# Kernel optimization log

Measured on AMD Instinct MI355X. Metric: run time of the kernel, lower is better.

## Reference

```python
import jax, jax.numpy as jnp
import numpy as np
import math

H, W = 1024, 1024

def setup_inputs() -> dict:
    key = jax.random.key(0)
    img = jax.random.uniform(key, (H, W), dtype=jnp.float32) * 255.0
    return {"InputImage": img}

def _phase_congruency(img):
    nrows, ncols = img.shape
    minWaveLength, mult = 3.0, 2.1
    nscale, norient = 5, 6
    sigmaOnf, k, cutOff, g = 0.55, 2.0, 0.5, 10.0
    eps = 1e-4

    cy, cx = nrows // 2, ncols // 2
    yy, xx = jnp.mgrid[0:nrows, 0:ncols]
    yy = (yy - cy) / nrows
    xx = (xx - cx) / ncols
    radius = jnp.sqrt(xx ** 2 + yy ** 2)
    radius = radius.at[cy, cx].set(1.0)
    theta = jnp.arctan2(-yy, xx)
    sintheta, costheta = jnp.sin(theta), jnp.cos(theta)

    # low-pass Butterworth (order 15, cutoff 0.45)
    normradius = radius / (jnp.abs(xx).max() * 2)
    lowpass = 1.0 / (1.0 + (normradius / 0.45) ** 30)

    # log-Gabor radial filters, [nscale, H, W]
    s = jnp.arange(nscale, dtype=jnp.float32)
    fo = 1.0 / (minWaveLength * mult ** s)            # [S]
    logGabor = jnp.exp(-jnp.log(radius[None] * (1.0 / fo)[:, None, None]) ** 2
                       / (2 * math.log(sigmaOnf) ** 2))
    annular = logGabor * lowpass[None]
    annular = annular.at[:, cy, cx].set(0.0)

    # angular spread, [norient, H, W]
    angl = jnp.arange(norient, dtype=jnp.float32) * (math.pi / norient)
    cosA, sinA = jnp.cos(angl), jnp.sin(angl)
    ds = sintheta[None] * cosA[:, None, None] - costheta[None] * sinA[:, None, None]
    dc = costheta[None] * cosA[:, None, None] + sintheta[None] * sinA[:, None, None]
    dtheta = jnp.minimum(jnp.abs(jnp.arctan2(ds, dc)) * (norient / 2), math.pi)
    spread = (jnp.cos(dtheta) + 1.0) / 2.0

    # full filter bank [O, S, H, W], shifted to DFT layout
    filt = jnp.fft.ifftshift(spread[:, None] * annular[None], axes=(-2, -1))

    F = jnp.fft.fft2(img)                              # complex64
    # cv2.idft is unscaled -> multiply numpy-style ifft by N
    z = jnp.fft.ifft2(filt * F[None, None]) * (nrows * ncols)   # [O,S,H,W]
    # original code: E (even) = channel 1 = Im(z), O (odd) = channel 0 = Re(z)
    E, O = z.imag, z.real
    An = jnp.abs(z)

    sumE = E.sum(axis=1)        # [O,H,W]
    sumO = O.sum(axis=1)
    sumAn = An.sum(axis=1)
    maxAn = An.max(axis=1)
    tau = jnp.median(An[:, 0].reshape(norient, -1), axis=1) / math.sqrt(math.log(4.0))

    XEnergy = jnp.sqrt(sumE ** 2 + sumO ** 2) + eps
    MeanE = sumE / XEnergy
    MeanO = sumO / XEnergy
    Energy = (E * MeanE[:, None] + O * MeanO[:, None]
              - jnp.abs(E * MeanO[:, None] - O * MeanE[:, None])).sum(axis=1)

    totalTau = tau * (1 - (1 / mult) ** nscale) / (1 - 1 / mult)   # [O]
    T = totalTau * math.sqrt(math.pi / 2) + k * totalTau * math.sqrt((4 - math.pi) / 2)
    Energy = jnp.maximum(Energy - T[:, None, None], 0.0)

    width = (sumAn / (maxAn + eps) - 1.0) / (nscale - 1)
    weight = 1.0 / (1.0 + jnp.exp((cutOff - width) * g))
    PC = weight * Energy / sumAn                       # [O,H,W]

    covx = PC * cosA[:, None, None]
    covy = PC * sinA[:, None, None]
    covx2 = (covx ** 2).sum(axis=0) / (norient / 2)
    covy2 = (covy ** 2).sum(axis=0) / (norient / 2)
    covxy = 4.0 * (covx * covy).sum(axis=0) / norient
    denom = jnp.sqrt(covxy ** 2 + (covx2 - covy2) ** 2) + eps
    M = (covy2 + covx2 + denom) / 2.0
    m = (covy2 + covx2 - denom) / 2.0
    return M, m

def reference(InputImage):
    M, m = _phase_congruency(InputImage)
    return (M, m)
```

## Files before the change

kernel.cpp:

```cpp
#include <hip/hip_runtime.h>
#include <math.h>

typedef float2 c2;

#define S_IDX(i) ((i) ^ (((i) >> 5) & 15))
#define SLAB_STRIDE 1025

__device__ __forceinline__ c2 cmul(c2 a, c2 b){
  return make_float2(a.x*b.x - a.y*b.y, a.x*b.y + a.y*b.x);
}

__constant__ float c_foinv[5] = {3.0f, 6.3f, 13.23f, 27.783f, 58.3443f};
__constant__ float c_lnfo[5]  = {1.0986123f, 1.8405496f, 2.5824700f, 3.3244106f, 4.0663219f};
__constant__ float c_angl[6]  = {0.0f, 0.5235988f, 1.0471976f, 1.5707963f, 2.0943951f, 2.6179939f};
__constant__ float c_cosA[6] = {1.0f, 0.8660254038f, 0.5f, 6.123233996e-17f, -0.5f, -0.8660254038f};
__constant__ float c_sinA[6] = {0.0f, 0.5f, 0.8660254038f, 1.0f, 0.8660254038f, 0.5f};

template<int SIGN>
__device__ __forceinline__ void make_tw(int t, c2* w){
#pragma unroll
  for (int k = 0; k < 5; ++k){
    const int s = 1 << (2*k);
    const float ang = (float)SIGN * 0.00613592315154256f * (float)(t & ~(s-1));
    sincosf(ang, &w[k].y, &w[k].x);
  }
}

template<int SIGN>
__device__ __forceinline__ void fft1024(c2* bufA, c2* bufB, int t, const c2* w){
  c2* cur = bufA; c2* oth = bufB;
#pragma unroll
  for (int k = 0; k < 5; ++k){
    const int s = 1 << (2*k);
    const int q = t & (s - 1);
    c2 a = cur[S_IDX(t)];
    c2 b = cur[S_IDX(t + 256)];
    c2 c = cur[S_IDX(t + 512)];
    c2 d = cur[S_IDX(t + 768)];
    c2 w1 = w[k];
    c2 w2 = cmul(w1, w1);
    c2 w3 = cmul(w2, w1);
    c2 apc = make_float2(a.x + c.x, a.y + c.y);
    c2 amc = make_float2(a.x - c.x, a.y - c.y);
    c2 bpd = make_float2(b.x + d.x, b.y + d.y);
    c2 bmd = make_float2(b.x - d.x, b.y - d.y);
    c2 y0 = make_float2(apc.x + bpd.x, apc.y + bpd.y);
    c2 e2 = make_float2(apc.x - bpd.x, apc.y - bpd.y);
    const float S4 = (float)SIGN;
    c2 u1 = make_float2(amc.x - S4*bmd.y, amc.y + S4*bmd.x);
    c2 u3 = make_float2(amc.x + S4*bmd.y, amc.y - S4*bmd.x);
    c2 y1 = cmul(u1, w1);
    c2 y2 = cmul(e2, w2);
    c2 y3 = cmul(u3, w3);
    const int bw = 4*t - 3*q;
    oth[S_IDX(bw)]       = y0;
    oth[S_IDX(bw + s)]   = y1;
    oth[S_IDX(bw + 2*s)] = y2;
    oth[S_IDX(bw + 3*s)] = y3;
    c2* tmp = cur; cur = oth; oth = tmp;
    __syncthreads();
  }
}

__device__ __forceinline__ float filt_eval(int c, int r, float yy,
                                           float cosA, float sinA, float foinv){
  const float xx = (float)(c < 512 ? c : c - 1024) * (1.0f/1024.0f);
  const bool isdc = (c == 0) && (r == 0);
  const float radius = isdc ? 1.0f : sqrtf(xx*xx + yy*yy);
  const float tt = radius * (1.0f/0.45f);
  const float t2 = tt*tt, t4 = t2*t2, t8 = t4*t4, t16 = t8*t8;
  const float lp = 1.0f / (1.0f + t16*t8*t4*t2);
  const float lnr = logf(radius * foinv);
  const float lg = expf(-lnr*lnr * 1.3989572f);
  const float ir = 1.0f / radius;
  const float st = -yy * ir, ct = xx * ir;
  const float dsv = st*cosA - ct*sinA;
  const float dcv = ct*cosA + st*sinA;
  const float dth = fminf(fabsf(atan2f(dsv, dcv)) * 3.0f, 3.14159274f);
  const float spr = 0.5f * (cosf(dth) + 1.0f);
  const float f = lg * lp * spr;
  return isdc ? 0.0f : f;
}

__global__ __launch_bounds__(256) void k_filt_tab(float* __restrict__ lnrT, float* __restrict__ thetaT){
  const int r = blockIdx.x;
  const int t = threadIdx.x;
  const float yy = (float)(r < 512 ? r : r - 1024) * (1.0f/1024.0f);
#pragma unroll
  for (int j = 0; j < 4; ++j){
    const int c = t + 256*j;
    const float xx = (float)(c < 512 ? c : c - 1024) * (1.0f/1024.0f);
    const float radius = sqrtf(xx*xx + yy*yy);
    float lnr = logf(radius);
    if (r == 0 && c == 0) lnr = __int_as_float(0x7F800000);
    lnrT[r*1024 + c] = lnr;
    thetaT[r*1024 + c] = atan2f(-yy, xx);
  }
}

__global__ __launch_bounds__(256) void k_fft_fwd_real(const float* __restrict__ in, c2* __restrict__ out){
  const int t = threadIdx.x;
  __shared__ c2 bufA[1024];
  __shared__ c2 bufB[1024];
  c2 w[5]; make_tw<-1>(t, w);
  for (int rr = 0; rr < 4; ++rr){
    const int row = blockIdx.x * 4 + rr;
    const float* src = in + (size_t)row * 1024;
    c2* dst = out + (size_t)row * 1024;
#pragma unroll
    for (int j = 0; j < 4; ++j){
      const int q = t + 256*j;
      bufA[S_IDX(q)] = make_float2(src[q], 0.0f);
    }
    __syncthreads();
    fft1024<-1>(bufA, bufB, t, w);
#pragma unroll
    for (int j = 0; j < 4; ++j){ const int q = t + 256*j; dst[q] = bufB[S_IDX(q)]; }
    __syncthreads();
  }
}

template<int SIGN>
__global__ __launch_bounds__(256) void k_fft_col_slab(c2* __restrict__ Z){
  __shared__ c2 slab[8 * SLAB_STRIDE];
  __shared__ c2 bufB[1024];
  c2* base = Z + (size_t)blockIdx.y * 1048576;
  const int t = threadIdx.x;
  const int col0 = blockIdx.x * 8;
  const int cl = t & 7;
  const int rw = t >> 3;
  c2 w[5]; make_tw<SIGN>(t, w);
  for (int ch = 0; ch < 32; ++ch){
    const int row = ch * 32 + rw;
    slab[cl * SLAB_STRIDE + S_IDX(row)] = base[(size_t)row * 1024 + col0 + cl];
  }
  __syncthreads();
  for (int c = 0; c < 8; ++c){
    c2* colp = slab + c * SLAB_STRIDE;
#pragma unroll
    for (int j = 0; j < 4; ++j) bufB[t + 256*j] = colp[t + 256*j];
    __syncthreads();
    fft1024<SIGN>(bufB, colp, t, w);
  }
  for (int ch = 0; ch < 32; ++ch){
    const int row = ch * 32 + rw;
    base[(size_t)row * 1024 + col0 + cl] = slab[cl * SLAB_STRIDE + S_IDX(row)];
  }
}

__global__ __launch_bounds__(256) void k_fft_inv_filter_t(const c2* __restrict__ F, c2* __restrict__ Z,
                                                          const float* __restrict__ lnrT,
                                                          const float* __restrict__ thetaT){
  const int t = threadIdx.x;
  const int gslot = blockIdx.y;
  const int orient = gslot / 5;
  const int scale = gslot - orient*5;
  const float lnfo = c_lnfo[scale];
  const float angl = c_angl[orient];
  __shared__ c2 bufA[1024];
  __shared__ c2 bufB[1024];
  c2 w[5]; make_tw<1>(t, w);
  for (int rr = 0; rr < 4; ++rr){
    const int row = blockIdx.x * 4 + rr;
    const c2* src = F + (size_t)row * 1024;
    const float* lnrR = lnrT + (size_t)row * 1024;
    const float* thR  = thetaT + (size_t)row * 1024;
    c2* dst = Z + (size_t)gslot * 1048576 + (size_t)row * 1024;
#pragma unroll
    for (int j = 0; j < 4; ++j){
      const int q = t + 256*j;
      const c2 v = src[q];
      const float lnr = lnrR[q];
      const float th  = thR[q];
      const float u = lnr + lnfo;
      const float lg = __expf(-u*u * 1.3989572f);
      const float lp = 1.0f / (1.0f + __expf(fmaf(30.0f, lnr, 23.955231f)));
      float d = th - angl;
      if (d <= -3.14159274f) d += 6.28318548f;
      const float dth = fminf(fabsf(d) * 3.0f, 3.14159274f);
      const float spr = 0.5f * (__cosf(dth) + 1.0f);
      const float f = lg * lp * spr;
      bufA[S_IDX(q)] = make_float2(v.x*f, v.y*f);
    }
    __syncthreads();
    fft1024<1>(bufA, bufB, t, w);
#pragma unroll
    for (int j = 0; j < 4; ++j){ const int q = t + 256*j; dst[q] = bufB[S_IDX(q)]; }
    __syncthreads();
  }
}

__global__ __launch_bounds__(256) void k_fft_inv_filter_b(const c2* __restrict__ F, c2* __restrict__ Z,
                                                          int slot0){
  const int t = threadIdx.x;
  const int gslot = slot0 + blockIdx.y;
  const int orient = gslot / 5;
  const int scale = gslot - orient*5;
  const float foinv = c_foinv[scale];
  const float cosA = c_cosA[orient], sinA = c_sinA[orient];
  __shared__ c2 bufA[1024];
  __shared__ c2 bufB[1024];
  c2 w[5]; make_tw<1>(t, w);
  for (int rr = 0; rr < 4; ++rr){
    const int row = blockIdx.x * 4 + rr;
    const c2* src = F + (size_t)row * 1024;
    c2* dst = Z + (size_t)blockIdx.y * 1048576 + (size_t)row * 1024;
    const float yy = (float)(row < 512 ? row : row - 1024) * (1.0f/1024.0f);
#pragma unroll
    for (int j = 0; j < 4; ++j){
      const int q = t + 256*j;
      const c2 v = src[q];
      const float f = filt_eval(q, row, yy, cosA, sinA, foinv);
      bufA[S_IDX(q)] = make_float2(v.x*f, v.y*f);
    }
    __syncthreads();
    fft1024<1>(bufA, bufB, t, w);
#pragma unroll
    for (int j = 0; j < 4; ++j){ const int q = t + 256*j; dst[q] = bufB[S_IDX(q)]; }
    __syncthreads();
  }
}


__device__ __forceinline__ unsigned amp_bits(const c2 v){
  return __float_as_uint(sqrtf(v.x*v.x + v.y*v.y));
}

__global__ __launch_bounds__(256) void k_med_p1b(const c2* __restrict__ Zb, size_t oStride,
                                                 unsigned* __restrict__ g1, int oBase){
  __shared__ unsigned h[4][4096];
  const int t = threadIdx.x;
  const int wv = t >> 6;
  const c2* z0 = Zb + (size_t)blockIdx.y * oStride;
  unsigned* gg = g1 + (size_t)(oBase + blockIdx.y) * 4096;
  for (int j = t; j < 4*4096; j += 256) ((unsigned*)h)[j] = 0;
  __syncthreads();
  const int base = blockIdx.x * 16384;
  for (int it = 0; it < 64; ++it){
    const unsigned bits = amp_bits(z0[base + it*256 + t]);
    atomicAdd(&h[wv][bits >> 20], 1u);
  }
  __syncthreads();
  for (int j = t; j < 4096; j += 256){
    const unsigned s = h[0][j] + h[1][j] + h[2][j] + h[3][j];
    if (s) atomicAdd(&gg[j], s);
  }
}

__global__ __launch_bounds__(256) void k_sel1b(const unsigned* __restrict__ g1,
                                               unsigned* __restrict__ sc1,
                                               unsigned* __restrict__ g2, int oBase){
  __shared__ unsigned partial[256];
  const int t = threadIdx.x;
  const int oo = oBase + blockIdx.x;
  const unsigned* gg = g1 + (size_t)oo * 4096;
  unsigned loc[16]; unsigned s = 0;
#pragma unroll
  for (int j = 0; j < 16; ++j){ loc[j] = gg[t*16 + j]; s += loc[j]; }
  partial[t] = s;
  __syncthreads();
  unsigned p = 0;
  for (int u = 0; u < t; ++u) p += partial[u];
  for (int which = 0; which < 2; ++which){
    const unsigned R = 524287u + (unsigned)which;
    if (R >= p && R - p < s){
      unsigned cum = p;
      for (int j = 0; j < 16; ++j){
        if (R - cum < loc[j]){ sc1[oo*4 + which*2] = (unsigned)(t*16 + j); sc1[oo*4 + which*2+1] = R - cum; break; }
        cum += loc[j];
      }
    }
  }
  for (int j = t; j < 8192; j += 256) g2[(size_t)oo*8192 + j] = 0;
}

__global__ __launch_bounds__(256) void k_med_p2b(const c2* __restrict__ Zb, size_t oStride,
                                                 const unsigned* __restrict__ sc1,
                                                 unsigned* __restrict__ g2, int oBase){
  __shared__ unsigned h[2][4096];
  const int t = threadIdx.x;
  const int oo = oBase + blockIdx.y;
  const c2* z0 = Zb + (size_t)blockIdx.y * oStride;
  unsigned* gg = g2 + (size_t)oo * 8192;
  for (int j = t; j < 8192; j += 256) ((unsigned*)h)[j] = 0;
  __syncthreads();
  const unsigned b0 = sc1[oo*4 + 0], b1 = sc1[oo*4 + 2];
  const int base = blockIdx.x * 16384;
  for (int it = 0; it < 64; ++it){
    const unsigned bits = amp_bits(z0[base + it*256 + t]);
    const unsigned top = bits >> 20;
    const unsigned mid = (bits >> 8) & 4095u;
    if (top == b0)      atomicAdd(&h[0][mid], 1u);
    else if (top == b1) atomicAdd(&h[1][mid], 1u);
  }
  __syncthreads();
  for (int j = t; j < 4096; j += 256){
    if (h[0][j]) atomicAdd(&gg[j], h[0][j]);
    if (h[1][j]) atomicAdd(&gg[4096 + j], h[1][j]);
  }
}

__global__ __launch_bounds__(256) void k_sel2b(const unsigned* __restrict__ g2,
                                               const unsigned* __restrict__ sc1,
                                               unsigned* __restrict__ sc2,
                                               unsigned* __restrict__ g3, int oBase){
  __shared__ unsigned partial[256];
  const int t = threadIdx.x;
  const int oo = oBase + blockIdx.x;
  const unsigned b0 = sc1[oo*4+0], lr0 = sc1[oo*4+1], b1 = sc1[oo*4+2], lr1 = sc1[oo*4+3];
  for (int which = 0; which < 2; ++which){
    const unsigned* hh = g2 + (size_t)oo*8192 + ((which == 1 && b1 != b0) ? 4096 : 0);
    const unsigned R = which ? lr1 : lr0;
    unsigned loc[16]; unsigned s = 0;
#pragma unroll
    for (int j = 0; j < 16; ++j){ loc[j] = hh[t*16 + j]; s += loc[j]; }
    partial[t] = s;
    __syncthreads();
    unsigned p = 0;
    for (int u = 0; u < t; ++u) p += partial[u];
    if (R >= p && R - p < s){
      unsigned cum = p;
      for (int j = 0; j < 16; ++j){
        if (R - cum < loc[j]){ sc2[oo*4 + which*2] = (unsigned)(t*16 + j); sc2[oo*4 + which*2+1] = R - cum; break; }
        cum += loc[j];
      }
    }
    __syncthreads();
  }
  for (int j = t; j < 512; j += 256) g3[(size_t)oo*512 + j] = 0;
}

__global__ __launch_bounds__(256) void k_med_p3b(const c2* __restrict__ Zb, size_t oStride,
                                                 const unsigned* __restrict__ sc1,
                                                 const unsigned* __restrict__ sc2,
                                                 unsigned* __restrict__ g3, int oBase){
  __shared__ unsigned h[2][256];
  const int t = threadIdx.x;
  const int oo = oBase + blockIdx.y;
  const c2* z0 = Zb + (size_t)blockIdx.y * oStride;
  unsigned* gg = g3 + (size_t)oo * 512;
  h[0][t] = 0; h[1][t] = 0;
  __syncthreads();
  const unsigned k0 = (sc1[oo*4+0] << 12) | sc2[oo*4+0];
  const unsigned k1 = (sc1[oo*4+2] << 12) | sc2[oo*4+2];
  const int base = blockIdx.x * 16384;
  for (int it = 0; it < 64; ++it){
    const unsigned bits = amp_bits(z0[base + it*256 + t]);
    const unsigned key = bits >> 8;
    if (key == k0)       atomicAdd(&h[0][bits & 255u], 1u);
    else if (key == k1)  atomicAdd(&h[1][bits & 255u], 1u);
  }
  __syncthreads();
  if (h[0][t]) atomicAdd(&gg[t], h[0][t]);
  if (h[1][t]) atomicAdd(&gg[256 + t], h[1][t]);
}

__global__ __launch_bounds__(256) void k_sel3b(const unsigned* __restrict__ g3,
                                               const unsigned* __restrict__ sc1,
                                               const unsigned* __restrict__ sc2,
                                               float* __restrict__ Tval, int oBase){
  __shared__ unsigned partial[256];
  __shared__ float vres[2];
  const int t = threadIdx.x;
  const int oo = oBase + blockIdx.x;
  const unsigned k0 = (sc1[oo*4+0] << 12) | sc2[oo*4+0];
  const unsigned k1 = (sc1[oo*4+2] << 12) | sc2[oo*4+2];
  for (int which = 0; which < 2; ++which){
    const unsigned* hh = g3 + (size_t)oo*512 + ((which == 1 && k1 != k0) ? 256 : 0);
    const unsigned R = which ? sc2[oo*4+3] : sc2[oo*4+1];
    partial[t] = hh[t];
    __syncthreads();
    unsigned p = 0;
    for (int u = 0; u < t; ++u) p += partial[u];
    if (R >= p && R - p < partial[t]){
      const unsigned key = which ? k1 : k0;
      vres[which] = __uint_as_float((key << 8) | (unsigned)t);
    }
    __syncthreads();
  }
  if (t == 0){
    const float med = 0.5f * (vres[0] + vres[1]);
    const float tau = med / 1.17741001f;
    const float totalTau = tau * 1.8623464f;
    const float T = totalTau * 1.25331414f + 2.0f * totalTau * 0.65513638f;
    Tval[oo] = T;
  }
}


__global__ __launch_bounds__(256) void k_pix_all(const c2* __restrict__ Z, const float* __restrict__ Tval,
                                                 float* __restrict__ out){
  const int i = blockIdx.x * 256 + threadIdx.x;
  float covx2 = 0.f, covy2 = 0.f, covxy = 0.f;
#pragma unroll
  for (int o = 0; o < 6; ++o){
    const float T = Tval[o];
    float E[5], O[5];
    float sumE = 0.f, sumO = 0.f, sumAn = 0.f, maxAn = 0.f;
#pragma unroll
    for (int s = 0; s < 5; ++s){
      const c2 z = Z[(size_t)(o*5 + s) * 1048576 + i];
      O[s] = z.x; E[s] = z.y;
      const float an = sqrtf(z.x*z.x + z.y*z.y);
      sumE += E[s]; sumO += O[s]; sumAn += an; maxAn = fmaxf(maxAn, an);
    }
    const float XE = sqrtf(sumE*sumE + sumO*sumO) + 1e-4f;
    const float ME = sumE / XE, MO = sumO / XE;
    float energy = 0.f;
#pragma unroll
    for (int s = 0; s < 5; ++s)
      energy += E[s]*ME + O[s]*MO - fabsf(E[s]*MO - O[s]*ME);
    energy = fmaxf(energy - T, 0.f);
    const float width = (sumAn / (maxAn + 1e-4f) - 1.0f) * 0.25f;
    const float weight = 1.0f / (1.0f + expf((0.5f - width) * 10.0f));
    const float PC = weight * energy / sumAn;
    const float cx = PC * c_cosA[o], cy = PC * c_sinA[o];
    covx2 += cx*cx; covy2 += cy*cy; covxy += cx*cy;
  }
  covx2 *= (1.0f/3.0f);
  covy2 *= (1.0f/3.0f);
  covxy *= (4.0f/6.0f);
  const float dnm = sqrtf(covxy*covxy + (covx2 - covy2)*(covx2 - covy2)) + 1e-4f;
  const float ss = covy2 + covx2;
  out[i] = (ss + dnm) / 2.0f;
  out[1048576 + i] = (ss - dnm) / 2.0f;
}


__global__ __launch_bounds__(256) void k_pix(const c2* __restrict__ Z, const float* __restrict__ Tp,
                                             float cA, float sA,
                                             float* __restrict__ ax2, float* __restrict__ ay2,
                                             float* __restrict__ axy, int first){
  const int i = blockIdx.x * 256 + threadIdx.x;
  const float T = *Tp;
  float E[5], O[5];
  float sumE = 0.f, sumO = 0.f, sumAn = 0.f, maxAn = 0.f;
#pragma unroll
  for (int s = 0; s < 5; ++s){
    const c2 z = Z[(size_t)s * 1048576 + i];
    O[s] = z.x; E[s] = z.y;
    const float an = sqrtf(z.x*z.x + z.y*z.y);
    sumE += E[s]; sumO += O[s]; sumAn += an; maxAn = fmaxf(maxAn, an);
  }
  const float XE = sqrtf(sumE*sumE + sumO*sumO) + 1e-4f;
  const float ME = sumE / XE, MO = sumO / XE;
  float energy = 0.f;
#pragma unroll
  for (int s = 0; s < 5; ++s)
    energy += E[s]*ME + O[s]*MO - fabsf(E[s]*MO - O[s]*ME);
  energy = fmaxf(energy - T, 0.f);
  const float width = (sumAn / (maxAn + 1e-4f) - 1.0f) * 0.25f;
  const float weight = 1.0f / (1.0f + expf((0.5f - width) * 10.0f));
  const float PC = weight * energy / sumAn;
  const float cx = PC * cA, cy = PC * sA;
  if (first){ ax2[i] = cx*cx; ay2[i] = cy*cy; axy[i] = cx*cy; }
  else      { ax2[i] += cx*cx; ay2[i] += cy*cy; axy[i] += cx*cy; }
}

__global__ __launch_bounds__(256) void k_final(const float* __restrict__ ax2, const float* __restrict__ ay2,
                                               const float* __restrict__ axy, float* __restrict__ out){
  const int i = blockIdx.x * 256 + threadIdx.x;
  const float cx2 = ax2[i] / 3.0f;
  const float cy2 = ay2[i] / 3.0f;
  const float cxy = 4.0f * axy[i] / 6.0f;
  const float dnm = sqrtf(cxy*cxy + (cx2 - cy2)*(cx2 - cy2)) + 1e-4f;
  const float ss = cy2 + cx2;
  out[i] = (ss + dnm) / 2.0f;
  out[1048576 + i] = (ss - dnm) / 2.0f;
}

extern "C" void kernel_launch(void* const* d_in, const int* in_sizes, int n_in,
                              void* d_out, int out_size, void* d_ws, size_t ws_size,
                              hipStream_t stream){
  (void)in_sizes; (void)n_in; (void)out_size;
  const float* img = (const float*)d_in[0];
  float* out = (float*)d_out;
  char* w = (char*)d_ws;

  const dim3 th(256);

  if (ws_size >= (size_t)268435456){
    c2* F  = (c2*)(w);
    c2* Z  = (c2*)(w + 8388608);
    float* lnrT   = (float*)(w + 260046848);
    float* thetaT = (float*)(w + 264241152);
    unsigned* g1  = (unsigned*)(w);
    unsigned* g2  = (unsigned*)(w + 98304);
    unsigned* g3  = (unsigned*)(w + 294912);
    unsigned* sc1 = (unsigned*)(w + 307200);
    unsigned* sc2 = (unsigned*)(w + 307328);
    float* Tval   = (float*)(w + 307456);

    k_filt_tab<<<dim3(1024), th, 0, stream>>>(lnrT, thetaT);

    k_fft_fwd_real<<<dim3(256), th, 0, stream>>>(img, F);
    k_fft_col_slab<-1><<<dim3(128, 1), th, 0, stream>>>(F);

    k_fft_inv_filter_t<<<dim3(256, 30), th, 0, stream>>>(F, Z, lnrT, thetaT);
    k_fft_col_slab<1><<<dim3(128, 30), th, 0, stream>>>(Z);

    hipMemsetAsync(g1, 0, 6*16384, stream);
    const size_t oStride = (size_t)5 * 1048576;
    k_med_p1b<<<dim3(64, 6), th, 0, stream>>>(Z, oStride, g1, 0);
    k_sel1b<<<dim3(6), th, 0, stream>>>(g1, sc1, g2, 0);
    k_med_p2b<<<dim3(64, 6), th, 0, stream>>>(Z, oStride, sc1, g2, 0);
    k_sel2b<<<dim3(6), th, 0, stream>>>(g2, sc1, sc2, g3, 0);
    k_med_p3b<<<dim3(64, 6), th, 0, stream>>>(Z, oStride, sc1, sc2, g3, 0);
    k_sel3b<<<dim3(6), th, 0, stream>>>(g3, sc1, sc2, Tval, 0);

    k_pix_all<<<dim3(4096), th, 0, stream>>>(Z, Tval, out);
  } else {
    c2* F   = (c2*)(w);
    c2* C5  = (c2*)(w + 8388608);
    float* ax2 = (float*)(w + 50331648);
    float* ay2 = ax2 + 1048576;
    float* axy = ay2 + 1048576;
    unsigned* g1  = (unsigned*)(w + 62914560);
    unsigned* g2  = (unsigned*)(w + 62930944);
    unsigned* g3  = (unsigned*)(w + 62963712);
    unsigned* sc1 = (unsigned*)(w + 62965760);
    unsigned* sc2 = (unsigned*)(w + 62965888);
    float* Tval   = (float*)(w + 62966016);

    k_fft_fwd_real<<<dim3(256), th, 0, stream>>>(img, F);
    k_fft_col_slab<-1><<<dim3(128, 1), th, 0, stream>>>(F);

    for (int o = 0; o < 6; ++o){
      k_fft_inv_filter_b<<<dim3(256, 5), th, 0, stream>>>(F, C5, o*5);
      k_fft_col_slab<1><<<dim3(128, 5), th, 0, stream>>>(C5);

      hipMemsetAsync(g1, 0, 16384, stream);
      k_med_p1b<<<dim3(64, 1), th, 0, stream>>>(C5, 0, g1, 0);
      k_sel1b<<<dim3(1), th, 0, stream>>>(g1, sc1, g2, 0);
      k_med_p2b<<<dim3(64, 1), th, 0, stream>>>(C5, 0, sc1, g2, 0);
      k_sel2b<<<dim3(1), th, 0, stream>>>(g2, sc1, sc2, g3, 0);
      k_med_p3b<<<dim3(64, 1), th, 0, stream>>>(C5, 0, sc1, sc2, g3, 0);
      k_sel3b<<<dim3(1), th, 0, stream>>>(g3, sc1, sc2, Tval, 0);

      const double a = (double)o * (M_PI/6.0);
      k_pix<<<dim3(4096), th, 0, stream>>>(C5, Tval, (float)cos(a), (float)sin(a),
                                           ax2, ay2, axy, (o == 0) ? 1 : 0);
    }
    k_final<<<dim3(4096), th, 0, stream>>>(ax2, ay2, axy, out);
  }
}
```

Measured before the change: 422.9 us.

## Replace radix-4 shared-memory FFT with register-resident 32x32 four-step FFT

Replaces the five-stage radix-4 shared-memory FFT, which needs a barrier per stage, with a four-step 32x32 decomposition. Each thread holds 32 elements in registers, runs a fully unrolled radix-2 FFT32 with constant twiddles, applies inner twiddles, and goes through one padded shared-memory transpose. Row and column kernels now each handle 8 lines per block in a padded slab, which cuts barriers and shared-memory traffic. The fallback path now also uses the precomputed filter tables. The cost is high register pressure (32 complex values per thread) and occupancy limited by launch bounds of 2.

```diff
diff --git a/kernel.cpp b/kernel.cpp
--- a/kernel.cpp
+++ b/kernel.cpp
@@ -3,83 +3,178 @@
 
 typedef float2 c2;
 
-#define S_IDX(i) ((i) ^ (((i) >> 5) & 15))
-#define SLAB_STRIDE 1025
+#define CSTR 1058
+#define POS(n) (33*((n)>>5) + ((n)&31))
 
 __device__ __forceinline__ c2 cmul(c2 a, c2 b){
   return make_float2(a.x*b.x - a.y*b.y, a.x*b.y + a.y*b.x);
 }
 
-__constant__ float c_foinv[5] = {3.0f, 6.3f, 13.23f, 27.783f, 58.3443f};
+__constant__ float2 c_tw32[16] = {
+  {1.0f, 0.0f},
+  {0.980785280f, 0.195090322f},
+  {0.923879533f, 0.382683432f},
+  {0.831469612f, 0.555570233f},
+  {0.707106781f, 0.707106781f},
+  {0.555570233f, 0.831469612f},
+  {0.382683432f, 0.923879533f},
+  {0.195090322f, 0.980785280f},
+  {0.0f, 1.0f},
+  {-0.195090322f, 0.980785280f},
+  {-0.382683432f, 0.923879533f},
+  {-0.555570233f, 0.831469612f},
+  {-0.707106781f, 0.707106781f},
+  {-0.831469612f, 0.555570233f},
+  {-0.923879533f, 0.382683432f},
+  {-0.980785280f, 0.195090322f}
+};
+
 __constant__ float c_lnfo[5]  = {1.0986123f, 1.8405496f, 2.5824700f, 3.3244106f, 4.0663219f};
 __constant__ float c_angl[6]  = {0.0f, 0.5235988f, 1.0471976f, 1.5707963f, 2.0943951f, 2.6179939f};
 __constant__ float c_cosA[6] = {1.0f, 0.8660254038f, 0.5f, 6.123233996e-17f, -0.5f, -0.8660254038f};
 __constant__ float c_sinA[6] = {0.0f, 0.5f, 0.8660254038f, 1.0f, 0.8660254038f, 0.5f};
 
+__device__ __forceinline__ constexpr int rev5(int k){
+  return ((k&1)<<4) | ((k&2)<<2) | (k&4) | ((k&8)>>2) | ((k>>4)&1);
+}
+
+template<int SIGN, int M>
+__device__ __forceinline__ void stage32(c2* r){
+#pragma unroll
+  for (int g = 0; g < 32; g += 2*M){
+#pragma unroll
+    for (int i = 0; i < M; ++i){
+      const c2 a = r[g+i], b = r[g+i+M];
+      r[g+i] = make_float2(a.x+b.x, a.y+b.y);
+      c2 d = make_float2(a.x-b.x, a.y-b.y);
+      if (i != 0){
+        const float2 tt = c_tw32[i*(16/M)];
+        d = cmul(d, make_float2(tt.x, (float)SIGN*tt.y));
+      }
+      r[g+i+M] = d;
+    }
+  }
+}
+
 template<int SIGN>
-__device__ __forceinline__ void make_tw(int t, c2* w){
-#pragma unroll
-  for (int k = 0; k < 5; ++k){
-    const int s = 1 << (2*k);
-    const float ang = (float)SIGN * 0.00613592315154256f * (float)(t & ~(s-1));
-    sincosf(ang, &w[k].y, &w[k].x);
-  }
+__device__ __forceinline__ void fft32(c2* r){
+  stage32<SIGN,16>(r);
+  stage32<SIGN,8>(r);
+  stage32<SIGN,4>(r);
+  stage32<SIGN,2>(r);
+  stage32<SIGN,1>(r);
 }
 
 template<int SIGN>
-__device__ __forceinline__ void fft1024(c2* bufA, c2* bufB, int t, const c2* w){
-  c2* cur = bufA; c2* oth = bufB;
-#pragma unroll
-  for (int k = 0; k < 5; ++k){
-    const int s = 1 << (2*k);
-    const int q = t & (s - 1);
-    c2 a = cur[S_IDX(t)];
-    c2 b = cur[S_IDX(t + 256)];
-    c2 c = cur[S_IDX(t + 512)];
-    c2 d = cur[S_IDX(t + 768)];
-    c2 w1 = w[k];
-    c2 w2 = cmul(w1, w1);
-    c2 w3 = cmul(w2, w1);
-    c2 apc = make_float2(a.x + c.x, a.y + c.y);
-    c2 amc = make_float2(a.x - c.x, a.y - c.y);
-    c2 bpd = make_float2(b.x + d.x, b.y + d.y);
-    c2 bmd = make_float2(b.x - d.x, b.y - d.y);
-    c2 y0 = make_float2(apc.x + bpd.x, apc.y + bpd.y);
-    c2 e2 = make_float2(apc.x - bpd.x, apc.y - bpd.y);
-    const float S4 = (float)SIGN;
-    c2 u1 = make_float2(amc.x - S4*bmd.y, amc.y + S4*bmd.x);
-    c2 u3 = make_float2(amc.x + S4*bmd.y, amc.y - S4*bmd.x);
-    c2 y1 = cmul(u1, w1);
-    c2 y2 = cmul(e2, w2);
-    c2 y3 = cmul(u3, w3);
-    const int bw = 4*t - 3*q;
-    oth[S_IDX(bw)]       = y0;
-    oth[S_IDX(bw + s)]   = y1;
-    oth[S_IDX(bw + 2*s)] = y2;
-    oth[S_IDX(bw + 3*s)] = y3;
-    c2* tmp = cur; cur = oth; oth = tmp;
-    __syncthreads();
-  }
-}
-
-__device__ __forceinline__ float filt_eval(int c, int r, float yy,
-                                           float cosA, float sinA, float foinv){
-  const float xx = (float)(c < 512 ? c : c - 1024) * (1.0f/1024.0f);
-  const bool isdc = (c == 0) && (r == 0);
-  const float radius = isdc ? 1.0f : sqrtf(xx*xx + yy*yy);
-  const float tt = radius * (1.0f/0.45f);
-  const float t2 = tt*tt, t4 = t2*t2, t8 = t4*t4, t16 = t8*t8;
-  const float lp = 1.0f / (1.0f + t16*t8*t4*t2);
-  const float lnr = logf(radius * foinv);
-  const float lg = expf(-lnr*lnr * 1.3989572f);
-  const float ir = 1.0f / radius;
-  const float st = -yy * ir, ct = xx * ir;
-  const float dsv = st*cosA - ct*sinA;
-  const float dcv = ct*cosA + st*sinA;
-  const float dth = fminf(fabsf(atan2f(dsv, dcv)) * 3.0f, 3.14159274f);
-  const float spr = 0.5f * (cosf(dth) + 1.0f);
-  const float f = lg * lp * spr;
-  return isdc ? 0.0f : f;
+__device__ void fft1024_4step(c2* slab, int t){
+  const int sub = t & 7;
+  const int idx = t >> 3;
+  c2* line = slab + sub*CSTR;
+  c2 r[32];
+#pragma unroll
+  for (int a = 0; a < 32; ++a) r[a] = line[33*a + idx];
+  fft32<SIGN>(r);
+  {
+    const float ang = (float)SIGN * 0.006135923151542565f * (float)idx;
+    c2 wst; sincosf(ang, &wst.y, &wst.x);
+    c2 wc = make_float2(1.f, 0.f);
+#pragma unroll
+    for (int d = 0; d < 32; ++d){
+      if ((d & 7) == 0 && d != 0){ float s, c; sincosf(ang*(float)d, &s, &c); wc = make_float2(c, s); }
+      c2 v = r[rev5(d)];
+      if (d != 0) v = cmul(v, wc);
+      line[33*d + idx] = v;
+      wc = cmul(wc, wst);
+    }
+  }
+  __syncthreads();
+#pragma unroll
+  for (int b = 0; b < 32; ++b) r[b] = line[33*idx + b];
+  __syncthreads();
+  fft32<SIGN>(r);
+#pragma unroll
+  for (int c = 0; c < 32; ++c) line[33*c + idx] = r[rev5(c)];
+}
+
+
+template<int SIGN>
+__global__ __launch_bounds__(256, 2) void k_col_fft(c2* __restrict__ Z){
+  __shared__ c2 slab[8*CSTR];
+  const int t = threadIdx.x;
+  c2* base = Z + (size_t)blockIdx.y * 1048576;
+  const int col0 = blockIdx.x * 8;
+  const int cl = t & 7, rw = t >> 3;
+#pragma unroll
+  for (int it = 0; it < 32; ++it){
+    const int row = it*32 + rw;
+    slab[cl*CSTR + 33*it + rw] = base[(size_t)row*1024 + col0 + cl];
+  }
+  __syncthreads();
+  fft1024_4step<SIGN>(slab, t);
+  __syncthreads();
+#pragma unroll
+  for (int it = 0; it < 32; ++it){
+    const int row = it*32 + rw;
+    base[(size_t)row*1024 + col0 + cl] = slab[cl*CSTR + 33*it + rw];
+  }
+}
+
+__global__ __launch_bounds__(256, 2) void k_row_fft_real(const float* __restrict__ in, c2* __restrict__ out){
+  __shared__ c2 slab[8*CSTR];
+  const int t = threadIdx.x;
+  const int row0 = blockIdx.x * 8;
+#pragma unroll
+  for (int it = 0; it < 32; ++it){
+    const int g = it*256 + t;
+    const int r = g >> 10, n = g & 1023;
+    slab[r*CSTR + POS(n)] = make_float2(in[(size_t)(row0+r)*1024 + n], 0.f);
+  }
+  __syncthreads();
+  fft1024_4step<-1>(slab, t);
+  __syncthreads();
+#pragma unroll
+  for (int it = 0; it < 32; ++it){
+    const int g = it*256 + t;
+    const int r = g >> 10, n = g & 1023;
+    out[(size_t)(row0+r)*1024 + n] = slab[r*CSTR + POS(n)];
+  }
+}
+
+__global__ __launch_bounds__(256, 2) void k_row_ifft_filter(const c2* __restrict__ F, c2* __restrict__ Z,
+                                                            const float* __restrict__ lnrT,
+                                                            const float* __restrict__ thetaT, int slot0){
+  __shared__ c2 slab[8*CSTR];
+  const int t = threadIdx.x;
+  const int gslot = slot0 + blockIdx.y;
+  const int orient = gslot / 5, scale = gslot - orient*5;
+  const float lnfo = c_lnfo[scale], angl = c_angl[orient];
+  const int row0 = blockIdx.x * 8;
+  c2* dst = Z + (size_t)blockIdx.y * 1048576;
+#pragma unroll
+  for (int it = 0; it < 32; ++it){
+    const int g = it*256 + t;
+    const int r = g >> 10, n = g & 1023;
+    const size_t gi = (size_t)(row0+r)*1024 + n;
+    const c2 v = F[gi];
+    const float lnr = lnrT[gi], th = thetaT[gi];
+    const float u = lnr + lnfo;
+    const float lg = __expf(-u*u*1.3989572f);
+    const float lp = 1.0f/(1.0f + __expf(fmaf(30.f, lnr, 23.955231f)));
+    float d = th - angl;
+    if (d <= -3.14159274f) d += 6.28318548f;
+    const float dth = fminf(fabsf(d)*3.0f, 3.14159274f);
+    const float f = lg*lp*0.5f*(__cosf(dth)+1.0f);
+    slab[r*CSTR + POS(n)] = make_float2(v.x*f, v.y*f);
+  }
+  __syncthreads();
+  fft1024_4step<1>(slab, t);
+  __syncthreads();
+#pragma unroll
+  for (int it = 0; it < 32; ++it){
+    const int g = it*256 + t;
+    const int r = g >> 10, n = g & 1023;
+    dst[(size_t)(row0+r)*1024 + n] = slab[r*CSTR + POS(n)];
+  }
 }
 
 __global__ __launch_bounds__(256) void k_filt_tab(float* __restrict__ lnrT, float* __restrict__ thetaT){
@@ -95,129 +190,6 @@
     if (r == 0 && c == 0) lnr = __int_as_float(0x7F800000);
     lnrT[r*1024 + c] = lnr;
     thetaT[r*1024 + c] = atan2f(-yy, xx);
-  }
-}
-
-__global__ __launch_bounds__(256) void k_fft_fwd_real(const float* __restrict__ in, c2* __restrict__ out){
-  const int t = threadIdx.x;
-  __shared__ c2 bufA[1024];
-  __shared__ c2 bufB[1024];
-  c2 w[5]; make_tw<-1>(t, w);
-  for (int rr = 0; rr < 4; ++rr){
-    const int row = blockIdx.x * 4 + rr;
-    const float* src = in + (size_t)row * 1024;
-    c2* dst = out + (size_t)row * 1024;
-#pragma unroll
-    for (int j = 0; j < 4; ++j){
-      const int q = t + 256*j;
-      bufA[S_IDX(q)] = make_float2(src[q], 0.0f);
-    }
-    __syncthreads();
-    fft1024<-1>(bufA, bufB, t, w);
-#pragma unroll
-    for (int j = 0; j < 4; ++j){ const int q = t + 256*j; dst[q] = bufB[S_IDX(q)]; }
-    __syncthreads();
-  }
-}
-
-template<int SIGN>
-__global__ __launch_bounds__(256) void k_fft_col_slab(c2* __restrict__ Z){
-  __shared__ c2 slab[8 * SLAB_STRIDE];
-  __shared__ c2 bufB[1024];
-  c2* base = Z + (size_t)blockIdx.y * 1048576;
-  const int t = threadIdx.x;
-  const int col0 = blockIdx.x * 8;
-  const int cl = t & 7;
-  const int rw = t >> 3;
-  c2 w[5]; make_tw<SIGN>(t, w);
-  for (int ch = 0; ch < 32; ++ch){
-    const int row = ch * 32 + rw;
-    slab[cl * SLAB_STRIDE + S_IDX(row)] = base[(size_t)row * 1024 + col0 + cl];
-  }
-  __syncthreads();
-  for (int c = 0; c < 8; ++c){
-    c2* colp = slab + c * SLAB_STRIDE;
-#pragma unroll
-    for (int j = 0; j < 4; ++j) bufB[t + 256*j] = colp[t + 256*j];
-    __syncthreads();
-    fft1024<SIGN>(bufB, colp, t, w);
-  }
-  for (int ch = 0; ch < 32; ++ch){
-    const int row = ch * 32 + rw;
-    base[(size_t)row * 1024 + col0 + cl] = slab[cl * SLAB_STRIDE + S_IDX(row)];
-  }
-}
-
-__global__ __launch_bounds__(256) void k_fft_inv_filter_t(const c2* __restrict__ F, c2* __restrict__ Z,
-                                                          const float* __restrict__ lnrT,
-                                                          const float* __restrict__ thetaT){
-  const int t = threadIdx.x;
-  const int gslot = blockIdx.y;
-  const int orient = gslot / 5;
-  const int scale = gslot - orient*5;
-  const float lnfo = c_lnfo[scale];
-  const float angl = c_angl[orient];
-  __shared__ c2 bufA[1024];
-  __shared__ c2 bufB[1024];
-  c2 w[5]; make_tw<1>(t, w);
-  for (int rr = 0; rr < 4; ++rr){
-    const int row = blockIdx.x * 4 + rr;
-    const c2* src = F + (size_t)row * 1024;
-    const float* lnrR = lnrT + (size_t)row * 1024;
-    const float* thR  = thetaT + (size_t)row * 1024;
-    c2* dst = Z + (size_t)gslot * 1048576 + (size_t)row * 1024;
-#pragma unroll
-    for (int j = 0; j < 4; ++j){
-      const int q = t + 256*j;
-      const c2 v = src[q];
-      const float lnr = lnrR[q];
-      const float th  = thR[q];
-      const float u = lnr + lnfo;
-      const float lg = __expf(-u*u * 1.3989572f);
-      const float lp = 1.0f / (1.0f + __expf(fmaf(30.0f, lnr, 23.955231f)));
-      float d = th - angl;
-      if (d <= -3.14159274f) d += 6.28318548f;
-      const float dth = fminf(fabsf(d) * 3.0f, 3.14159274f);
-      const float spr = 0.5f * (__cosf(dth) + 1.0f);
-      const float f = lg * lp * spr;
-      bufA[S_IDX(q)] = make_float2(v.x*f, v.y*f);
-    }
-    __syncthreads();
-    fft1024<1>(bufA, bufB, t, w);
-#pragma unroll
-    for (int j = 0; j < 4; ++j){ const int q = t + 256*j; dst[q] = bufB[S_IDX(q)]; }
-    __syncthreads();
-  }
-}
-
-__global__ __launch_bounds__(256) void k_fft_inv_filter_b(const c2* __restrict__ F, c2* __restrict__ Z,
-                                                          int slot0){
-  const int t = threadIdx.x;
-  const int gslot = slot0 + blockIdx.y;
-  const int orient = gslot / 5;
-  const int scale = gslot - orient*5;
-  const float foinv = c_foinv[scale];
-  const float cosA = c_cosA[orient], sinA = c_sinA[orient];
-  __shared__ c2 bufA[1024];
-  __shared__ c2 bufB[1024];
-  c2 w[5]; make_tw<1>(t, w);
-  for (int rr = 0; rr < 4; ++rr){
-    const int row = blockIdx.x * 4 + rr;
-    const c2* src = F + (size_t)row * 1024;
-    c2* dst = Z + (size_t)blockIdx.y * 1048576 + (size_t)row * 1024;
-    const float yy = (float)(row < 512 ? row : row - 1024) * (1.0f/1024.0f);
-#pragma unroll
-    for (int j = 0; j < 4; ++j){
-      const int q = t + 256*j;
-      const c2 v = src[q];
-      const float f = filt_eval(q, row, yy, cosA, sinA, foinv);
-      bufA[S_IDX(q)] = make_float2(v.x*f, v.y*f);
-    }
-    __syncthreads();
-    fft1024<1>(bufA, bufB, t, w);
-#pragma unroll
-    for (int j = 0; j < 4; ++j){ const int q = t + 256*j; dst[q] = bufB[S_IDX(q)]; }
-    __syncthreads();
   }
 }
 
@@ -493,11 +465,11 @@
 
     k_filt_tab<<<dim3(1024), th, 0, stream>>>(lnrT, thetaT);
 
-    k_fft_fwd_real<<<dim3(256), th, 0, stream>>>(img, F);
-    k_fft_col_slab<-1><<<dim3(128, 1), th, 0, stream>>>(F);
-
-    k_fft_inv_filter_t<<<dim3(256, 30), th, 0, stream>>>(F, Z, lnrT, thetaT);
-    k_fft_col_slab<1><<<dim3(128, 30), th, 0, stream>>>(Z);
+    k_row_fft_real<<<dim3(128), th, 0, stream>>>(img, F);
+    k_col_fft<-1><<<dim3(128, 1), th, 0, stream>>>(F);
+
+    k_row_ifft_filter<<<dim3(128, 30), th, 0, stream>>>(F, Z, lnrT, thetaT, 0);
+    k_col_fft<1><<<dim3(128, 30), th, 0, stream>>>(Z);
 
     hipMemsetAsync(g1, 0, 6*16384, stream);
     const size_t oStride = (size_t)5 * 1048576;
@@ -512,22 +484,25 @@
   } else {
     c2* F   = (c2*)(w);
     c2* C5  = (c2*)(w + 8388608);
-    float* ax2 = (float*)(w + 50331648);
+    float* lnrT   = (float*)(w + 50331648);
+    float* thetaT = (float*)(w + 54525952);
+    float* ax2 = (float*)(w + 58720256);
     float* ay2 = ax2 + 1048576;
     float* axy = ay2 + 1048576;
-    unsigned* g1  = (unsigned*)(w + 62914560);
-    unsigned* g2  = (unsigned*)(w + 62930944);
-    unsigned* g3  = (unsigned*)(w + 62963712);
-    unsigned* sc1 = (unsigned*)(w + 62965760);
-    unsigned* sc2 = (unsigned*)(w + 62965888);
-    float* Tval   = (float*)(w + 62966016);
-
-    k_fft_fwd_real<<<dim3(256), th, 0, stream>>>(img, F);
-    k_fft_col_slab<-1><<<dim3(128, 1), th, 0, stream>>>(F);
+    unsigned* g1  = (unsigned*)(w + 71303168);
+    unsigned* g2  = (unsigned*)(w + 71319552);
+    unsigned* g3  = (unsigned*)(w + 71352320);
+    unsigned* sc1 = (unsigned*)(w + 71354368);
+    unsigned* sc2 = (unsigned*)(w + 71354496);
+    float* Tval   = (float*)(w + 71354624);
+
+    k_filt_tab<<<dim3(1024), th, 0, stream>>>(lnrT, thetaT);
+    k_row_fft_real<<<dim3(128), th, 0, stream>>>(img, F);
+    k_col_fft<-1><<<dim3(128, 1), th, 0, stream>>>(F);
 
     for (int o = 0; o < 6; ++o){
-      k_fft_inv_filter_b<<<dim3(256, 5), th, 0, stream>>>(F, C5, o*5);
-      k_fft_col_slab<1><<<dim3(128, 5), th, 0, stream>>>(C5);
+      k_row_ifft_filter<<<dim3(128, 5), th, 0, stream>>>(F, C5, lnrT, thetaT, o*5);
+      k_col_fft<1><<<dim3(128, 5), th, 0, stream>>>(C5);
 
       hipMemsetAsync(g1, 0, 16384, stream);
       k_med_p1b<<<dim3(64, 1), th, 0, stream>>>(C5, 0, g1, 0);
```

Result: slower. 460.4 us (+8.9%).
